# Optimization experiments

Hardware: AMD Instinct MI355X
Metric: run time of the kernel (lower is better)

Reference implementation:

```python
import jax, jax.numpy as jnp
import numpy as np

N = 50000; E = 800000; G = 256; F = 34; D = 128; H = 4; C = 32; L = 4
EPS = 1e-5

def _bn(x, g, b):
    # BatchNorm1d with batch statistics (train-mode math), eval dropout (identity)
    m = jnp.mean(x, 0); v = jnp.var(x, 0)
    return g * (x - m) * jax.lax.rsqrt(v + EPS) + b

def _seg_softmax(s, seg, n):
    # numerically-stable softmax over edges grouped by destination node
    m = jax.ops.segment_max(s, seg, num_segments=n)
    m = jnp.where(jnp.isfinite(m), m, 0.0)
    e = jnp.exp(s - m[seg])
    d = jax.ops.segment_sum(e, seg, num_segments=n)
    return e / (d[seg] + 1e-16)

def setup_inputs():
    key = jax.random.key(0)
    ks = iter(jax.random.split(key, 64))
    def rn(shape, s=0.05):
        return jax.random.normal(next(ks), shape, dtype=jnp.float32) * s
    inp = {}
    inp['x'] = jax.random.normal(next(ks), (N, F), dtype=jnp.float32)
    inp['edge_index'] = jax.random.randint(next(ks), (2, E), 0, N, dtype=jnp.int32)
    inp['batch'] = jnp.sort(jax.random.randint(next(ks), (N,), 0, G, dtype=jnp.int32))
    inp['emb_W'] = rn((F, D)); inp['emb_b'] = rn((D,))
    inp['emb_g'] = jnp.ones((D,)); inp['emb_be'] = jnp.zeros((D,))
    inp['gWl'] = rn((L, D, D)); inp['gWr'] = rn((L, D, D))
    inp['gbl'] = rn((L, D)); inp['gbr'] = rn((L, D))
    inp['gatt'] = rn((L, H, C)); inp['gbias'] = rn((L, D))
    inp['gg'] = jnp.ones((L, D)); inp['gbe'] = jnp.zeros((L, D))
    inp['tWq'] = rn((D, D)); inp['tWk'] = rn((D, D)); inp['tWv'] = rn((D, D)); inp['tWs'] = rn((D, D))
    inp['tbq'] = rn((D,)); inp['tbk'] = rn((D,)); inp['tbv'] = rn((D,)); inp['tbs'] = rn((D,))
    inp['tg'] = jnp.ones((D,)); inp['tbe'] = jnp.zeros((D,))
    inp['oW1'] = rn((2 * D, D)); inp['ob1'] = rn((D,))
    inp['og'] = jnp.ones((D,)); inp['obe'] = jnp.zeros((D,))
    inp['oW2'] = rn((D, D // 2)); inp['ob2'] = rn((D // 2,))
    inp['oW3'] = rn((D // 2, 1)); inp['ob3'] = rn((1,))
    return inp

def reference(x, edge_index, batch, emb_W, emb_b, emb_g, emb_be, gWl, gWr, gbl, gbr, gatt, gbias, gg, gbe, tWq, tWk, tWv, tWs, tbq, tbk, tbv, tbs, tg, tbe, oW1, ob1, og, obe, oW2, ob2, oW3, ob3):
    x = jax.nn.relu(_bn(x @ emb_W + emb_b, emb_g, emb_be))
    sl = jnp.arange(N, dtype=edge_index.dtype)
    ei = jnp.concatenate([edge_index, jnp.stack([sl, sl])], axis=1)  # GATv2 default add_self_loops=True
    src, dst = ei[0], ei[1]
    for l in range(L):  # 4 structurally identical GATv2 layers
        xl = (x @ gWl[l] + gbl[l]).reshape(N, H, C)
        xr = (x @ gWr[l] + gbr[l]).reshape(N, H, C)
        e = jax.nn.leaky_relu(xl[src] + xr[dst], 0.2)  # [E+N, H, C]
        sc = jnp.einsum('ehc,hc->eh', e, gatt[l])
        a = _seg_softmax(sc, dst, N)
        out = jax.ops.segment_sum(xl[src] * a[..., None], dst, num_segments=N).reshape(N, D) + gbias[l]
        x = x + jax.nn.relu(_bn(out, gg[l], gbe[l]))
    # TransformerConv: no self-loops by default, dot-product attention + root skip
    s2, d2 = edge_index[0], edge_index[1]
    q = (x @ tWq + tbq).reshape(N, H, C)
    k = (x @ tWk + tbk).reshape(N, H, C)
    v = (x @ tWv + tbv).reshape(N, H, C)
    sc = jnp.einsum('ehc,ehc->eh', q[d2], k[s2]) / np.float32(np.sqrt(C))
    a = _seg_softmax(sc, d2, N)
    agg = jax.ops.segment_sum(v[s2] * a[..., None], d2, num_segments=N).reshape(N, D)
    x = x + _bn(agg + x @ tWs + tbs, tg, tbe)
    # global mean + max pooling over graphs
    cnt = jax.ops.segment_sum(jnp.ones((N,), x.dtype), batch, num_segments=G)
    xm = jax.ops.segment_sum(x, batch, num_segments=G) / jnp.maximum(cnt, 1.0)[:, None]
    xx = jax.ops.segment_max(x, batch, num_segments=G)
    xx = jnp.where(jnp.isfinite(xx), xx, 0.0)  # guard empty segments
    h = jnp.concatenate([xm, xx], axis=1)
    h = jax.nn.relu(_bn(h @ oW1 + ob1, og, obe))
    h = jax.nn.relu(h @ oW2 + ob2)
    return h @ oW3 + ob3
```

## Files before the change

### kernel.cpp

```cpp
#include <hip/hip_runtime.h>
#include <hip/hip_fp16.h>

namespace {
constexpr int NN = 50000;
constexpr int NE = 800000;
constexpr int NG = 256;
constexpr int NF = 34;
constexpr int NL = 4;
constexpr int NB = (NN + 255) / 256;
constexpr int STS = 32;
}
#define EPSB 1e-5f
#define LSLOPE 0.2f
#define INV_SQRT_C 0.17677669529663687f

typedef short bf16x8 __attribute__((ext_vector_type(8)));
typedef float f32x4 __attribute__((ext_vector_type(4)));
typedef _Float16 hv2 __attribute__((ext_vector_type(2)));

static __device__ __forceinline__ short f2bf(float f) {
    unsigned int u = __float_as_uint(f);
    u = (u + 0x7fff + ((u >> 16) & 1)) >> 16;
    return (short)u;
}
static __device__ __forceinline__ unsigned fenc(float x) {
    unsigned u = __float_as_uint(x);
    return (u & 0x80000000u) ? ~u : (u | 0x80000000u);
}
static __device__ __forceinline__ float fdec(unsigned u) {
    return __uint_as_float((u & 0x80000000u) ? (u ^ 0x80000000u) : ~u);
}
static __device__ __forceinline__ float fdot2(hv2 a, hv2 b, float c) {
    return __builtin_amdgcn_fdot2(a, b, c, false);
}

__global__ __launch_bounds__(256) void k_deg(const int* __restrict__ ei,
                                             int* __restrict__ deg,
                                             int* __restrict__ rank) {
    int tid = blockIdx.x * 256 + threadIdx.x;
    const int S = (NE + 3) / 4;
    if (tid >= S) return;
#pragma unroll
    for (int k = 0; k < 4; ++k) {
        int e = tid + k * S;
        if (e < NE) rank[e] = atomicAdd(&deg[ei[NE + e]], 1);
    }
}

__global__ __launch_bounds__(256) void k_scan1(const int* __restrict__ deg, int* __restrict__ bsum) {
    __shared__ int sm[256];
    int i = blockIdx.x * 256 + threadIdx.x;
    sm[threadIdx.x] = (i < NN) ? deg[i] : 0;
    __syncthreads();
    for (int off = 128; off > 0; off >>= 1) {
        if (threadIdx.x < off) sm[threadIdx.x] += sm[threadIdx.x + off];
        __syncthreads();
    }
    if (threadIdx.x == 0) bsum[blockIdx.x] = sm[0];
}

__global__ __launch_bounds__(256) void k_scan2(const int* __restrict__ bsum,
                                               int* __restrict__ boff, int* __restrict__ rp) {
    __shared__ int sm[256];
    int t = threadIdx.x;
    int v = (t < NB) ? bsum[t] : 0;
    sm[t] = v;
    __syncthreads();
    for (int off = 1; off < 256; off <<= 1) {
        int u = (t >= off) ? sm[t - off] : 0;
        __syncthreads();
        sm[t] += u;
        __syncthreads();
    }
    if (t < NB) boff[t] = sm[t] - v;
    if (t == 255) rp[NN] = sm[255];
}

__global__ __launch_bounds__(256) void k_scan3(const int* __restrict__ deg,
                                               const int* __restrict__ boff,
                                               int* __restrict__ rp) {
    __shared__ int sm[256];
    int i = blockIdx.x * 256 + threadIdx.x;
    int t = threadIdx.x;
    int v = (i < NN) ? deg[i] : 0;
    sm[t] = v;
    __syncthreads();
    for (int off = 1; off < 256; off <<= 1) {
        int u = (t >= off) ? sm[t - off] : 0;
        __syncthreads();
        sm[t] += u;
        __syncthreads();
    }
    if (i < NN) rp[i] = boff[blockIdx.x] + sm[t] - v;
}

__global__ __launch_bounds__(256) void k_fill(const int* __restrict__ ei,
                                              const int* __restrict__ rp,
                                              const int* __restrict__ rank,
                                              int* __restrict__ esrc) {
    int tid = blockIdx.x * 256 + threadIdx.x;
    const int S = (NE + 3) / 4;
    if (tid >= S) return;
#pragma unroll
    for (int k = 0; k < 4; ++k) {
        int e = tid + k * S;
        if (e < NE) {
            int s = ei[e];
            int d = ei[NE + e];
            int p = rp[d] + rank[e];
            esrc[p] = s;
        }
    }
}

__global__ __launch_bounds__(256) void k_prep(const float* __restrict__ gWl,
                                              const float* __restrict__ gWr,
                                              const float* __restrict__ tWq,
                                              const float* __restrict__ tWk,
                                              const float* __restrict__ tWv,
                                              const float* __restrict__ tWs,
                                              short* __restrict__ dst) {
    int m = blockIdx.x;
    const float* src;
    if (m < 4) src = gWl + m * 16384;
    else if (m < 8) src = gWr + (m - 4) * 16384;
    else if (m == 8) src = tWq;
    else if (m == 9) src = tWk;
    else if (m == 10) src = tWv;
    else src = tWs;
    short* d = dst + m * 16384;
    for (int i = threadIdx.x; i < 16384; i += 256) {
        int n = i >> 7, k = i & 127;
        d[i] = f2bf(src[k * 128 + n]);
    }
}

__global__ __launch_bounds__(256) void k_stats(const float* __restrict__ src, int nRows,
                                               float* __restrict__ st) {
    int c = threadIdx.x & 127;
    int sub = threadIdx.x >> 7;
    int r0 = blockIdx.x * 128;
    int rend = r0 + 128; if (rend > nRows) rend = nRows;
    float s = 0.f, ss = 0.f;
    for (int r = r0 + sub; r < rend; r += 2) {
        float v = src[(size_t)r * 128 + c];
        s += v; ss += v * v;
    }
    float* dst = st + (blockIdx.x & (STS - 1)) * 256;
    atomicAdd(&dst[c], s);
    atomicAdd(&dst[128 + c], ss);
}

template <int OUTH0, int OUTH1, int RES, int XOUT>
__global__ __launch_bounds__(256) void k_gemm2bn(const float* __restrict__ src,
                                                 const float* __restrict__ res,
                                                 float* __restrict__ xout,
                                                 const float* __restrict__ st,
                                                 const float* __restrict__ g,
                                                 const float* __restrict__ b,
                                                 const short* __restrict__ Wt0,
                                                 const short* __restrict__ Wt1,
                                                 const float* __restrict__ bias0,
                                                 const float* __restrict__ bias1,
                                                 void* __restrict__ out0,
                                                 void* __restrict__ out1, int nRows) {
    __shared__ short As[128 * 136];
    __shared__ short Bs[128 * 136];
    __shared__ float scsh[256];
    const float invn = 1.f / NN;
    if (threadIdx.x < 128) {
        int c = threadIdx.x;
        float s0v = 0.f, s1v = 0.f;
#pragma unroll 8
        for (int k2 = 0; k2 < STS; ++k2) {
            s0v += st[k2 * 256 + c];
            s1v += st[k2 * 256 + 128 + c];
        }
        float mean = s0v * invn;
        float var = fmaxf(s1v * invn - mean * mean, 0.f);
        float s = g[c] * rsqrtf(var + EPSB);
        scsh[c] = s;
        scsh[128 + c] = b[c] - mean * s;
    }
    {
        const int4* Wt4 = (const int4*)Wt0;
        for (int idx = threadIdx.x; idx < 2048; idx += 256) {
            int row = idx >> 4, c8 = idx & 15;
            *(int4*)&Bs[row * 136 + c8 * 8] = Wt4[idx];
        }
    }
    __syncthreads();
    int r0 = blockIdx.x * 128;
    int rows = nRows - r0; if (rows > 128) rows = 128;
    for (int idx = threadIdx.x; idx < 2048; idx += 256) {
        int r = idx >> 4, c8 = idx & 15;
        short4 sa = {0, 0, 0, 0}, sb = {0, 0, 0, 0};
        if (r < rows) {
            size_t base = (size_t)(r0 + r) * 128 + c8 * 8;
            float4 v0 = *(const float4*)&src[base];
            float4 v1 = *(const float4*)&src[base + 4];
            int c = c8 * 8;
            v0.x = fmaxf(v0.x * scsh[c + 0] + scsh[128 + c + 0], 0.f);
            v0.y = fmaxf(v0.y * scsh[c + 1] + scsh[128 + c + 1], 0.f);
            v0.z = fmaxf(v0.z * scsh[c + 2] + scsh[128 + c + 2], 0.f);
            v0.w = fmaxf(v0.w * scsh[c + 3] + scsh[128 + c + 3], 0.f);
            v1.x = fmaxf(v1.x * scsh[c + 4] + scsh[128 + c + 4], 0.f);
            v1.y = fmaxf(v1.y * scsh[c + 5] + scsh[128 + c + 5], 0.f);
            v1.z = fmaxf(v1.z * scsh[c + 6] + scsh[128 + c + 6], 0.f);
            v1.w = fmaxf(v1.w * scsh[c + 7] + scsh[128 + c + 7], 0.f);
            if (RES) {
                float4 rr0 = *(const float4*)&res[base];
                float4 rr1 = *(const float4*)&res[base + 4];
                v0.x += rr0.x; v0.y += rr0.y; v0.z += rr0.z; v0.w += rr0.w;
                v1.x += rr1.x; v1.y += rr1.y; v1.z += rr1.z; v1.w += rr1.w;
            }
            if (XOUT) {
                *(float4*)&xout[base] = v0;
                *(float4*)&xout[base + 4] = v1;
            }
            sa.x = f2bf(v0.x); sa.y = f2bf(v0.y); sa.z = f2bf(v0.z); sa.w = f2bf(v0.w);
            sb.x = f2bf(v1.x); sb.y = f2bf(v1.y); sb.z = f2bf(v1.z); sb.w = f2bf(v1.w);
        }
        *(short4*)&As[r * 136 + c8 * 8] = sa;
        *(short4*)&As[r * 136 + c8 * 8 + 4] = sb;
    }
    __syncthreads();
    int lane = threadIdx.x & 63, wave = threadIdx.x >> 6;
    int n16 = lane & 15, quad = lane >> 4;
    bf16x8 af[2][4];
#pragma unroll
    for (int rt = 0; rt < 2; ++rt)
#pragma unroll
        for (int kc = 0; kc < 4; ++kc)
            af[rt][kc] = *(const bf16x8*)&As[(wave * 32 + rt * 16 + n16) * 136 + kc * 32 + quad * 8];

    f32x4 acc[2][8];
#pragma unroll
    for (int rt = 0; rt < 2; ++rt)
#pragma unroll
        for (int ct = 0; ct < 8; ++ct) acc[rt][ct] = (f32x4){0.f, 0.f, 0.f, 0.f};
#pragma unroll
    for (int ct = 0; ct < 8; ++ct)
#pragma unroll
        for (int kc = 0; kc < 4; ++kc) {
            bf16x8 bf = *(const bf16x8*)&Bs[(ct * 16 + n16) * 136 + kc * 32 + quad * 8];
            acc[0][ct] = __builtin_amdgcn_mfma_f32_16x16x32_bf16(af[0][kc], bf, acc[0][ct], 0, 0, 0);
            acc[1][ct] = __builtin_amdgcn_mfma_f32_16x16x32_bf16(af[1][kc], bf, acc[1][ct], 0, 0, 0);
        }
#pragma unroll
    for (int ct = 0; ct < 8; ++ct) {
        int colI = ct * 16 + n16;
        float bv = bias0[colI];
#pragma unroll
        for (int rt = 0; rt < 2; ++rt)
#pragma unroll
            for (int reg = 0; reg < 4; ++reg) {
                int r = wave * 32 + rt * 16 + quad * 4 + reg;
                if (r < rows) {
                    float v = acc[rt][ct][reg] + bv;
                    if (OUTH0) ((__half*)out0)[(size_t)(r0 + r) * 128 + colI] = __float2half(v);
                    else       ((float*)out0)[(size_t)(r0 + r) * 128 + colI] = v;
                }
            }
    }
    __syncthreads();
    {
        const int4* Wt4 = (const int4*)Wt1;
        for (int idx = threadIdx.x; idx < 2048; idx += 256) {
            int row = idx >> 4, c8 = idx & 15;
            *(int4*)&Bs[row * 136 + c8 * 8] = Wt4[idx];
        }
    }
    __syncthreads();
#pragma unroll
    for (int rt = 0; rt < 2; ++rt)
#pragma unroll
        for (int ct = 0; ct < 8; ++ct) acc[rt][ct] = (f32x4){0.f, 0.f, 0.f, 0.f};
#pragma unroll
    for (int ct = 0; ct < 8; ++ct)
#pragma unroll
        for (int kc = 0; kc < 4; ++kc) {
            bf16x8 bf = *(const bf16x8*)&Bs[(ct * 16 + n16) * 136 + kc * 32 + quad * 8];
            acc[0][ct] = __builtin_amdgcn_mfma_f32_16x16x32_bf16(af[0][kc], bf, acc[0][ct], 0, 0, 0);
            acc[1][ct] = __builtin_amdgcn_mfma_f32_16x16x32_bf16(af[1][kc], bf, acc[1][ct], 0, 0, 0);
        }
#pragma unroll
    for (int ct = 0; ct < 8; ++ct) {
        int colI = ct * 16 + n16;
        float bv = bias1[colI];
#pragma unroll
        for (int rt = 0; rt < 2; ++rt)
#pragma unroll
            for (int reg = 0; reg < 4; ++reg) {
                int r = wave * 32 + rt * 16 + quad * 4 + reg;
                if (r < rows) {
                    float v = acc[rt][ct][reg] + bv;
                    if (OUTH1) ((__half*)out1)[(size_t)(r0 + r) * 128 + colI] = __float2half(v);
                    else       ((float*)out1)[(size_t)(r0 + r) * 128 + colI] = v;
                }
            }
    }
}

__global__ __launch_bounds__(256) void k_gemm4bn(const float* __restrict__ src,
                                                 const float* __restrict__ res,
                                                 float* __restrict__ xout,
                                                 const float* __restrict__ st,
                                                 const float* __restrict__ g,
                                                 const float* __restrict__ b,
                                                 const short* __restrict__ Wt,
                                                 const float* __restrict__ bq,
                                                 const float* __restrict__ bk,
                                                 const float* __restrict__ bv,
                                                 const float* __restrict__ bs,
                                                 __half* __restrict__ oq,
                                                 __half* __restrict__ ok,
                                                 __half* __restrict__ ov,
                                                 __half* __restrict__ os, int nRows) {
    __shared__ short As[128 * 136];
    __shared__ short Bs[128 * 136];
    __shared__ float scsh[256];
    const float invn = 1.f / NN;
    if (threadIdx.x < 128) {
        int c = threadIdx.x;
        float s0v = 0.f, s1v = 0.f;
#pragma unroll 8
        for (int k2 = 0; k2 < STS; ++k2) {
            s0v += st[k2 * 256 + c];
            s1v += st[k2 * 256 + 128 + c];
        }
        float mean = s0v * invn;
        float var = fmaxf(s1v * invn - mean * mean, 0.f);
        float s = g[c] * rsqrtf(var + EPSB);
        scsh[c] = s;
        scsh[128 + c] = b[c] - mean * s;
    }
    __syncthreads();
    int r0 = blockIdx.x * 128;
    int rows = nRows - r0; if (rows > 128) rows = 128;
    for (int idx = threadIdx.x; idx < 2048; idx += 256) {
        int r = idx >> 4, c8 = idx & 15;
        short4 sa = {0, 0, 0, 0}, sb = {0, 0, 0, 0};
        if (r < rows) {
            size_t base = (size_t)(r0 + r) * 128 + c8 * 8;
            float4 v0 = *(const float4*)&src[base];
            float4 v1 = *(const float4*)&src[base + 4];
            int c = c8 * 8;
            v0.x = fmaxf(v0.x * scsh[c + 0] + scsh[128 + c + 0], 0.f);
            v0.y = fmaxf(v0.y * scsh[c + 1] + scsh[128 + c + 1], 0.f);
            v0.z = fmaxf(v0.z * scsh[c + 2] + scsh[128 + c + 2], 0.f);
            v0.w = fmaxf(v0.w * scsh[c + 3] + scsh[128 + c + 3], 0.f);
            v1.x = fmaxf(v1.x * scsh[c + 4] + scsh[128 + c + 4], 0.f);
            v1.y = fmaxf(v1.y * scsh[c + 5] + scsh[128 + c + 5], 0.f);
            v1.z = fmaxf(v1.z * scsh[c + 6] + scsh[128 + c + 6], 0.f);
            v1.w = fmaxf(v1.w * scsh[c + 7] + scsh[128 + c + 7], 0.f);
            float4 rr0 = *(const float4*)&res[base];
            float4 rr1 = *(const float4*)&res[base + 4];
            v0.x += rr0.x; v0.y += rr0.y; v0.z += rr0.z; v0.w += rr0.w;
            v1.x += rr1.x; v1.y += rr1.y; v1.z += rr1.z; v1.w += rr1.w;
            *(float4*)&xout[base] = v0;
            *(float4*)&xout[base + 4] = v1;
            sa.x = f2bf(v0.x); sa.y = f2bf(v0.y); sa.z = f2bf(v0.z); sa.w = f2bf(v0.w);
            sb.x = f2bf(v1.x); sb.y = f2bf(v1.y); sb.z = f2bf(v1.z); sb.w = f2bf(v1.w);
        }
        *(short4*)&As[r * 136 + c8 * 8] = sa;
        *(short4*)&As[r * 136 + c8 * 8 + 4] = sb;
    }
    int lane = threadIdx.x & 63, wave = threadIdx.x >> 6;
    int n16 = lane & 15, quad = lane >> 4;
    __half* outs[4] = {oq, ok, ov, os};
    const float* biases[4] = {bq, bk, bv, bs};
    bf16x8 af[2][4];
    bool afLoaded = false;
    for (int m = 0; m < 4; ++m) {
        {
            const int4* Wt4 = (const int4*)(Wt + (size_t)m * 16384);
            for (int idx = threadIdx.x; idx < 2048; idx += 256) {
                int row = idx >> 4, c8 = idx & 15;
                *(int4*)&Bs[row * 136 + c8 * 8] = Wt4[idx];
            }
        }
        __syncthreads();
        if (!afLoaded) {
            afLoaded = true;
#pragma unroll
            for (int rt = 0; rt < 2; ++rt)
#pragma unroll
                for (int kc = 0; kc < 4; ++kc)
                    af[rt][kc] = *(const bf16x8*)&As[(wave * 32 + rt * 16 + n16) * 136 + kc * 32 + quad * 8];
        }
        f32x4 acc[2][8];
#pragma unroll
        for (int rt = 0; rt < 2; ++rt)
#pragma unroll
            for (int ct = 0; ct < 8; ++ct) acc[rt][ct] = (f32x4){0.f, 0.f, 0.f, 0.f};
#pragma unroll
        for (int ct = 0; ct < 8; ++ct)
#pragma unroll
            for (int kc = 0; kc < 4; ++kc) {
                bf16x8 bf = *(const bf16x8*)&Bs[(ct * 16 + n16) * 136 + kc * 32 + quad * 8];
                acc[0][ct] = __builtin_amdgcn_mfma_f32_16x16x32_bf16(af[0][kc], bf, acc[0][ct], 0, 0, 0);
                acc[1][ct] = __builtin_amdgcn_mfma_f32_16x16x32_bf16(af[1][kc], bf, acc[1][ct], 0, 0, 0);
            }
        __half* om = outs[m];
        const float* bm = biases[m];
#pragma unroll
        for (int ct = 0; ct < 8; ++ct) {
            int colI = ct * 16 + n16;
            float bv2 = bm[colI];
#pragma unroll
            for (int rt = 0; rt < 2; ++rt)
#pragma unroll
                for (int reg = 0; reg < 4; ++reg) {
                    int r = wave * 32 + rt * 16 + quad * 4 + reg;
                    if (r < rows)
                        om[(size_t)(r0 + r) * 128 + colI] = __float2half(acc[rt][ct][reg] + bv2);
                }
        }
        if (m < 3) __syncthreads();
    }
}

__global__ __launch_bounds__(256) void k_gemm_emb(const float* __restrict__ A,
                                                  const float* __restrict__ W,
                                                  const float* __restrict__ bias,
                                                  float* __restrict__ out, int nRows,
                                                  float* __restrict__ stms) {
    __shared__ float As[64 * NF];
    __shared__ float sred[256];
    int r0 = blockIdx.x * 64;
    int rows = nRows - r0; if (rows > 64) rows = 64;
    int total = rows * NF;
    for (int idx = threadIdx.x; idx < 64 * NF; idx += 256)
        As[idx] = (idx < total) ? A[(size_t)r0 * NF + idx] : 0.f;
    sred[threadIdx.x] = 0.f;
    __syncthreads();
    int tx = threadIdx.x & 31, ty = threadIdx.x >> 5;
    const float4* W4 = (const float4*)W;
    float acc[8][4];
#pragma unroll
    for (int j = 0; j < 8; ++j)
#pragma unroll
        for (int i = 0; i < 4; ++i) acc[j][i] = 0.f;
#pragma unroll 2
    for (int k = 0; k < NF; ++k) {
        float4 w = W4[k * 32 + tx];
#pragma unroll
        for (int j = 0; j < 8; ++j) {
            float a = As[(ty * 8 + j) * NF + k];
            acc[j][0] += a * w.x; acc[j][1] += a * w.y;
            acc[j][2] += a * w.z; acc[j][3] += a * w.w;
        }
    }
    float4 b = ((const float4*)bias)[tx];
    float s[4] = {0.f, 0.f, 0.f, 0.f}, ss[4] = {0.f, 0.f, 0.f, 0.f};
#pragma unroll
    for (int j = 0; j < 8; ++j) {
        int r = ty * 8 + j;
        if (r < rows) {
            float4 o = make_float4(acc[j][0] + b.x, acc[j][1] + b.y,
                                   acc[j][2] + b.z, acc[j][3] + b.w);
            ((float4*)out)[(size_t)(r0 + r) * 32 + tx] = o;
            s[0] += o.x; ss[0] += o.x * o.x;
            s[1] += o.y; ss[1] += o.y * o.y;
            s[2] += o.z; ss[2] += o.z * o.z;
            s[3] += o.w; ss[3] += o.w * o.w;
        }
    }
#pragma unroll
    for (int i = 0; i < 4; ++i) {
        atomicAdd(&sred[tx * 4 + i], s[i]);
        atomicAdd(&sred[128 + tx * 4 + i], ss[i]);
    }
    __syncthreads();
    atomicAdd(&stms[(blockIdx.x & (STS - 1)) * 256 + threadIdx.x], sred[threadIdx.x]);
}

__global__ __launch_bounds__(256) void k_gat_aggr(const __half* __restrict__ xl,
                                                  const __half* __restrict__ xr,
                                                  const float* __restrict__ att,
                                                  const float* __restrict__ gbias_l,
                                                  const int* __restrict__ rp,
                                                  const int* __restrict__ esrc,
                                                  float* __restrict__ out) {
    int lane = threadIdx.x & 63;
    int node = blockIdx.x * 4 + (threadIdx.x >> 6);
    if (node >= NN) return;
    int q = lane >> 4;
    int l16 = lane & 15;
    int c8 = l16 * 8;
    float4 xrr = *(const float4*)&xr[(unsigned)node * 128u + c8];
    hv2 xrh[4] = {*(hv2*)&xrr.x, *(hv2*)&xrr.y, *(hv2*)&xrr.z, *(hv2*)&xrr.w};
    float4 atA = *(const float4*)&att[c8];
    float4 atB = *(const float4*)&att[c8 + 4];
    hv2 ath[4] = {{(_Float16)atA.x, (_Float16)atA.y}, {(_Float16)atA.z, (_Float16)atA.w},
                  {(_Float16)atB.x, (_Float16)atB.y}, {(_Float16)atB.z, (_Float16)atB.w}};
    const hv2 hz = {(_Float16)0.f, (_Float16)0.f};
    const hv2 hs = {(_Float16)LSLOPE, (_Float16)LSLOPE};
    int s0 = rp[node];
    int T = rp[node + 1] - s0 + 1;
    float a[8] = {0.f, 0.f, 0.f, 0.f, 0.f, 0.f, 0.f, 0.f};
    float l = 0.f;
    auto body = [&](int j) {
        bool self = (j == T - 1);
        int srcn = self ? node : esrc[s0 + j];
        float4 raw = *(const float4*)&xl[(unsigned)srcn * 128u + c8];
        hv2 f[4] = {*(hv2*)&raw.x, *(hv2*)&raw.y, *(hv2*)&raw.z, *(hv2*)&raw.w};
        float p = 0.f;
#pragma unroll
        for (int k = 0; k < 4; ++k) {
            hv2 e = f[k] + xrh[k];
            hv2 lk = __builtin_elementwise_max(e, hz) + hs * __builtin_elementwise_min(e, hz);
            p = fdot2(lk, ath[k], p);
        }
        p += __shfl_xor(p, 1); p += __shfl_xor(p, 2);
        float w = __expf(p);
#pragma unroll
        for (int k = 0; k < 4; ++k) {
            a[2 * k] += w * (float)f[k].x;
            a[2 * k + 1] += w * (float)f[k].y;
        }
        l += w;
    };
    int j = q;
    for (; j + 12 < T; j += 16) { body(j); body(j + 4); body(j + 8); body(j + 12); }
    for (; j + 4 < T; j += 8) { body(j); body(j + 4); }
    for (; j < T; j += 4) body(j);
#pragma unroll
    for (int k = 0; k < 8; ++k) { a[k] += __shfl_xor(a[k], 16); a[k] += __shfl_xor(a[k], 32); }
    l += __shfl_xor(l, 16); l += __shfl_xor(l, 32);
    if (q == 0) {
        float inv = 1.f / (l + 1e-16f);
        float4 gb0 = *(const float4*)&gbias_l[c8];
        float4 gb1 = *(const float4*)&gbias_l[c8 + 4];
        float4 o0 = make_float4(a[0] * inv + gb0.x, a[1] * inv + gb0.y,
                                a[2] * inv + gb0.z, a[3] * inv + gb0.w);
        float4 o1 = make_float4(a[4] * inv + gb1.x, a[5] * inv + gb1.y,
                                a[6] * inv + gb1.z, a[7] * inv + gb1.w);
        *(float4*)&out[(unsigned)node * 128u + c8] = o0;
        *(float4*)&out[(unsigned)node * 128u + c8 + 4] = o1;
    }
}

__global__ __launch_bounds__(256) void k_trans_aggr(const __half* __restrict__ qh,
                                                    const __half* __restrict__ kh,
                                                    const __half* __restrict__ vv,
                                                    const __half* __restrict__ sT,
                                                    const int* __restrict__ rp,
                                                    const int* __restrict__ esrc,
                                                    float* __restrict__ out) {
    int lane = threadIdx.x & 63;
    int node = blockIdx.x * 4 + (threadIdx.x >> 6);
    if (node >= NN) return;
    int q = lane >> 4;
    int l16 = lane & 15;
    int c8 = l16 * 8;
    float4 qr = *(const float4*)&qh[(unsigned)node * 128u + c8];
    const hv2 hinv = {(_Float16)INV_SQRT_C, (_Float16)INV_SQRT_C};
    hv2 qv[4] = {(*(hv2*)&qr.x) * hinv, (*(hv2*)&qr.y) * hinv,
                 (*(hv2*)&qr.z) * hinv, (*(hv2*)&qr.w) * hinv};
    int s0 = rp[node];
    int T = rp[node + 1] - s0;
    float a[8] = {0.f, 0.f, 0.f, 0.f, 0.f, 0.f, 0.f, 0.f};
    float l = 0.f;
    auto body = [&](int j) {
        int srcn = esrc[s0 + j];
        float4 kraw = *(const float4*)&kh[(unsigned)srcn * 128u + c8];
        float4 vraw = *(const float4*)&vv[(unsigned)srcn * 128u + c8];
        hv2 kv[4] = {*(hv2*)&kraw.x, *(hv2*)&kraw.y, *(hv2*)&kraw.z, *(hv2*)&kraw.w};
        float p = 0.f;
#pragma unroll
        for (int k = 0; k < 4; ++k) p = fdot2(kv[k], qv[k], p);
        p += __shfl_xor(p, 1); p += __shfl_xor(p, 2);
        float w = __expf(p);
        hv2 vvv[4] = {*(hv2*)&vraw.x, *(hv2*)&vraw.y, *(hv2*)&vraw.z, *(hv2*)&vraw.w};
#pragma unroll
        for (int k = 0; k < 4; ++k) {
            a[2 * k] += w * (float)vvv[k].x;
            a[2 * k + 1] += w * (float)vvv[k].y;
        }
        l += w;
    };
    int j = q;
    for (; j + 12 < T; j += 16) { body(j); body(j + 4); body(j + 8); body(j + 12); }
    for (; j + 4 < T; j += 8) { body(j); body(j + 4); }
    for (; j < T; j += 4) body(j);
#pragma unroll
    for (int k = 0; k < 8; ++k) { a[k] += __shfl_xor(a[k], 16); a[k] += __shfl_xor(a[k], 32); }
    l += __shfl_xor(l, 16); l += __shfl_xor(l, 32);
    if (q == 0) {
        float inv = 1.f / (l + 1e-16f);
        float4 straw = *(const float4*)&sT[(unsigned)node * 128u + c8];
        hv2 st[4] = {*(hv2*)&straw.x, *(hv2*)&straw.y, *(hv2*)&straw.z, *(hv2*)&straw.w};
        float4 o0 = make_float4(a[0] * inv + (float)st[0].x, a[1] * inv + (float)st[0].y,
                                a[2] * inv + (float)st[1].x, a[3] * inv + (float)st[1].y);
        float4 o1 = make_float4(a[4] * inv + (float)st[2].x, a[5] * inv + (float)st[2].y,
                                a[6] * inv + (float)st[3].x, a[7] * inv + (float)st[3].y);
        *(float4*)&out[(unsigned)node * 128u + c8] = o0;
        *(float4*)&out[(unsigned)node * 128u + c8 + 4] = o1;
    }
}

__global__ __launch_bounds__(256) void k_pool_part(const float* __restrict__ src,
                                                   const float* __restrict__ res,
                                                   const float* __restrict__ st,
                                                   const float* __restrict__ g,
                                                   const float* __restrict__ b,
                                                   const int* __restrict__ batch,
                                                   float* __restrict__ psum,
                                                   unsigned* __restrict__ pmax) {
    __shared__ int bs[64];
    __shared__ float sc_sh[128], sh_sh[128];
    int r0 = blockIdx.x * 64;
    if (threadIdx.x < 64) {
        int r = r0 + threadIdx.x;
        bs[threadIdx.x] = (r < NN) ? batch[r] : -1;
    }
    const float invn = 1.f / NN;
    if (threadIdx.x < 128) {
        int c2 = threadIdx.x;
        float s0v = 0.f, s1v = 0.f;
#pragma unroll 8
        for (int k2 = 0; k2 < STS; ++k2) {
            s0v += st[k2 * 256 + c2];
            s1v += st[k2 * 256 + 128 + c2];
        }
        float mean = s0v * invn;
        float var = fmaxf(s1v * invn - mean * mean, 0.f);
        float scv = g[c2] * rsqrtf(var + EPSB);
        sc_sh[c2] = scv;
        sh_sh[c2] = b[c2] - mean * scv;
    }
    __syncthreads();
    int c = threadIdx.x & 127;
    int sub = threadIdx.x >> 7;
    float scv = sc_sh[c];
    float shv = sh_sh[c];
    int curg = -1;
    float s = 0.f, fmx = -INFINITY;
    for (int i = sub; i < 64; i += 2) {
        int r = r0 + i;
        if (r >= NN) break;
        int gr = bs[i];
        if (gr != curg) {
            if (curg >= 0) {
                atomicAdd(&psum[curg * 128 + c], s);
                atomicMax(&pmax[curg * 128 + c], fenc(fmx));
            }
            curg = gr; s = 0.f; fmx = -INFINITY;
        }
        float v = src[(size_t)r * 128 + c] * scv + shv + res[(size_t)r * 128 + c];
        s += v; fmx = fmaxf(fmx, v);
    }
    if (curg >= 0) {
        atomicAdd(&psum[curg * 128 + c], s);
        atomicMax(&pmax[curg * 128 + c], fenc(fmx));
    }
}

__global__ __launch_bounds__(128) void k_pool_head1(const float* __restrict__ psum,
                                                    const unsigned* __restrict__ pmax,
                                                    const int* __restrict__ batch,
                                                    const float* __restrict__ W,
                                                    const float* __restrict__ b,
                                                    float* __restrict__ t1,
                                                    float* __restrict__ st6) {
    __shared__ float hr[256];
    __shared__ int se[2];
    int g = blockIdx.x;
    int t = threadIdx.x;
    if (t == 0) {
        int lo = 0, hi = NN;
        while (lo < hi) { int mid = (lo + hi) >> 1; if (batch[mid] < g) lo = mid + 1; else hi = mid; }
        se[0] = lo;
        hi = NN;
        while (lo < hi) { int mid = (lo + hi) >> 1; if (batch[mid] < g + 1) lo = mid + 1; else hi = mid; }
        se[1] = lo;
    }
    __syncthreads();
    int cnt = se[1] - se[0];
    float xm = psum[g * 128 + t] / fmaxf((float)cnt, 1.f);
    float xx = (cnt > 0) ? fdec(pmax[g * 128 + t]) : 0.f;
    hr[t] = xm;
    hr[128 + t] = xx;
    __syncthreads();
    float acc = b[t];
#pragma unroll 4
    for (int k = 0; k < 256; ++k) acc += hr[k] * W[k * 128 + t];
    t1[g * 128 + t] = acc;
    atomicAdd(&st6[t], acc);
    atomicAdd(&st6[128 + t], acc * acc);
}

__global__ __launch_bounds__(64) void k_head2(const float* __restrict__ t1,
                                              const float* __restrict__ st,
                                              const float* __restrict__ og,
                                              const float* __restrict__ obe,
                                              const float* __restrict__ W2,
                                              const float* __restrict__ b2,
                                              const float* __restrict__ W3,
                                              const float* __restrict__ b3,
                                              float* __restrict__ out) {
    __shared__ float v[128];
    int row = blockIdx.x, t = threadIdx.x;
    const float invn = 1.f / NG;
#pragma unroll
    for (int half = 0; half < 2; ++half) {
        int ch = t + half * 64;
        float mean = st[ch] * invn;
        float var = fmaxf(st[128 + ch] * invn - mean * mean, 0.f);
        float scv = og[ch] * rsqrtf(var + EPSB);
        float shv = obe[ch] - mean * scv;
        float a = t1[row * 128 + ch] * scv + shv;
        v[ch] = fmaxf(a, 0.f);
    }
    __syncthreads();
    float acc = b2[t];
#pragma unroll 4
    for (int k = 0; k < 128; ++k) acc += v[k] * W2[k * 64 + t];
    float p = fmaxf(acc, 0.f) * W3[t];
    p += __shfl_xor(p, 1); p += __shfl_xor(p, 2); p += __shfl_xor(p, 4);
    p += __shfl_xor(p, 8); p += __shfl_xor(p, 16); p += __shfl_xor(p, 32);
    if (t == 0) out[row] = p + b3[0];
}

extern "C" void kernel_launch(void* const* d_in, const int* in_sizes, int n_in,
                              void* d_out, int out_size, void* d_ws, size_t ws_size,
                              hipStream_t stream) {
    const float* x_in   = (const float*)d_in[0];
    const int*   ei     = (const int*)d_in[1];
    const int*   batch  = (const int*)d_in[2];
    const float* emb_W  = (const float*)d_in[3];
    const float* emb_b  = (const float*)d_in[4];
    const float* emb_g  = (const float*)d_in[5];
    const float* emb_be = (const float*)d_in[6];
    const float* gWl    = (const float*)d_in[7];
    const float* gWr    = (const float*)d_in[8];
    const float* gbl    = (const float*)d_in[9];
    const float* gbr    = (const float*)d_in[10];
    const float* gatt   = (const float*)d_in[11];
    const float* gbias  = (const float*)d_in[12];
    const float* gg     = (const float*)d_in[13];
    const float* gbe    = (const float*)d_in[14];
    const float* tWq    = (const float*)d_in[15];
    const float* tWk    = (const float*)d_in[16];
    const float* tWv    = (const float*)d_in[17];
    const float* tWs    = (const float*)d_in[18];
    const float* tbq    = (const float*)d_in[19];
    const float* tbk    = (const float*)d_in[20];
    const float* tbv    = (const float*)d_in[21];
    const float* tbs    = (const float*)d_in[22];
    const float* tg     = (const float*)d_in[23];
    const float* tbe    = (const float*)d_in[24];
    const float* oW1    = (const float*)d_in[25];
    const float* ob1    = (const float*)d_in[26];
    const float* og     = (const float*)d_in[27];
    const float* obe    = (const float*)d_in[28];
    const float* oW2    = (const float*)d_in[29];
    const float* ob2    = (const float*)d_in[30];
    const float* oW3    = (const float*)d_in[31];
    const float* ob3    = (const float*)d_in[32];
    float* out = (float*)d_out;

    const size_t NDsz = (size_t)NN * 128;
    float* x     = (float*)d_ws;
    float* bA    = x + NDsz;
    float* bC    = bA + NDsz;
    float* stats = bC + NDsz;
    float* hpool = stats + 7 * 256;
    float* t1    = hpool + 65536;
    float* scb   = t1 + 32768;
    __half* xlh  = (__half*)(scb + (size_t)(NE + NN) * 4);
    __half* xrh  = xlh + NDsz;
    __half* vh   = xrh + NDsz;
    __half* sh   = vh + NDsz;
    short* Wt    = (short*)(sh + NDsz);
    int* deg     = (int*)(Wt + 12 * 16384);
    int* rp      = deg + NN;
    int* cursor  = rp + NN + 1;
    int2* edg    = (int2*)(cursor + NN);
    int* bsum    = (int*)(edg + NE + 64);
    int* boff    = bsum + 256;
    float* psum  = (float*)(boff + 256);
    unsigned* pmax = (unsigned*)(psum + NG * 128);
    int* rank    = (int*)scb;
    int* esrc    = (int*)edg;
    float* stms  = scb + NE;

    hipMemsetAsync(deg, 0, NN * sizeof(int), stream);
    hipMemsetAsync(stats + 6 * 256, 0, 256 * sizeof(float), stream);
    hipMemsetAsync(stms, 0, 6 * STS * 256 * sizeof(float), stream);
    hipMemsetAsync(psum, 0, NG * 128 * 2 * sizeof(float), stream);

    k_prep<<<12, 256, 0, stream>>>(gWl, gWr, tWq, tWk, tWv, tWs, Wt);

    const int S4 = (NE + 3) / 4;
    const int gQuarter = (S4 + 255) / 256;
    k_deg<<<gQuarter, 256, 0, stream>>>(ei, deg, rank);
    k_scan1<<<NB, 256, 0, stream>>>(deg, bsum);
    k_scan2<<<1, 256, 0, stream>>>(bsum, boff, rp);
    k_scan3<<<NB, 256, 0, stream>>>(deg, boff, rp);
    k_fill<<<gQuarter, 256, 0, stream>>>(ei, rp, rank, esrc);

    const int gEmb  = (NN + 63) / 64;
    const int gGemm = (NN + 127) / 128;
    const int gStat = (NN + 127) / 128;
    const int gNode = (NN + 3) / 4;
    const int gPool = (NN + 63) / 64;
    const int REG = STS * 256;

    k_gemm_emb<<<gEmb, 256, 0, stream>>>(x_in, emb_W, emb_b, bA, NN, stms + 0 * REG);

    k_gemm2bn<1, 1, 0, 1><<<gGemm, 256, 0, stream>>>(bA, nullptr, x, stms + 0 * REG, emb_g, emb_be,
                                                     Wt + (size_t)0 * 16384, Wt + (size_t)4 * 16384,
                                                     gbl + 0 * 128, gbr + 0 * 128, xlh, xrh, NN);
    k_gat_aggr<<<gNode, 256, 0, stream>>>(xlh, xrh, gatt + 0 * 128, gbias + 0 * 128, rp, esrc, bC);
    k_stats<<<gStat, 256, 0, stream>>>(bC, NN, stms + 1 * REG);
    k_gemm2bn<1, 1, 1, 1><<<gGemm, 256, 0, stream>>>(bC, x, bA, stms + 1 * REG, gg + 0 * 128, gbe + 0 * 128,
                                                     Wt + (size_t)1 * 16384, Wt + (size_t)5 * 16384,
                                                     gbl + 1 * 128, gbr + 1 * 128, xlh, xrh, NN);
    k_gat_aggr<<<gNode, 256, 0, stream>>>(xlh, xrh, gatt + 1 * 128, gbias + 1 * 128, rp, esrc, bC);
    k_stats<<<gStat, 256, 0, stream>>>(bC, NN, stms + 2 * REG);
    k_gemm2bn<1, 1, 1, 1><<<gGemm, 256, 0, stream>>>(bC, bA, x, stms + 2 * REG, gg + 1 * 128, gbe + 1 * 128,
                                                     Wt + (size_t)2 * 16384, Wt + (size_t)6 * 16384,
                                                     gbl + 2 * 128, gbr + 2 * 128, xlh, xrh, NN);
    k_gat_aggr<<<gNode, 256, 0, stream>>>(xlh, xrh, gatt + 2 * 128, gbias + 2 * 128, rp, esrc, bC);
    k_stats<<<gStat, 256, 0, stream>>>(bC, NN, stms + 3 * REG);
    k_gemm2bn<1, 1, 1, 1><<<gGemm, 256, 0, stream>>>(bC, x, bA, stms + 3 * REG, gg + 2 * 128, gbe + 2 * 128,
                                                     Wt + (size_t)3 * 16384, Wt + (size_t)7 * 16384,
                                                     gbl + 3 * 128, gbr + 3 * 128, xlh, xrh, NN);
    k_gat_aggr<<<gNode, 256, 0, stream>>>(xlh, xrh, gatt + 3 * 128, gbias + 3 * 128, rp, esrc, bC);
    k_stats<<<gStat, 256, 0, stream>>>(bC, NN, stms + 4 * REG);

    k_gemm4bn<<<gGemm, 256, 0, stream>>>(bC, bA, x, stms + 4 * REG, gg + 3 * 128, gbe + 3 * 128,
                                         Wt + (size_t)8 * 16384, tbq, tbk, tbv, tbs,
                                         xrh, xlh, vh, sh, NN);
    k_trans_aggr<<<gNode, 256, 0, stream>>>(xrh, xlh, vh, sh, rp, esrc, bC);
    k_stats<<<gStat, 256, 0, stream>>>(bC, NN, stms + 5 * REG);

    k_pool_part<<<gPool, 256, 0, stream>>>(bC, x, stms + 5 * REG, tg, tbe, batch, psum, pmax);
    k_pool_head1<<<NG, 128, 0, stream>>>(psum, pmax, batch, oW1, ob1, t1, stats + 6 * 256);
    k_head2<<<NG, 64, 0, stream>>>(t1, stats + 6 * 256, og, obe, oW2, ob2, oW3, ob3, out);
}
```

Baseline: 821.8 us.

## Merge init kernels into one launch and widen per-lane columns in edge aggregation

Degree counting, weight transpose/conversion and the embedding GEMM are combined into a single kernel, with each block picking its role from its block index. This removes two launches and lets the independent pieces run concurrently. The GAT and Transformer aggregation kernels now give each lane 16 columns instead of 8, so 8 edges are processed in parallel per wave instead of 4. That halves the shuffles in the score reduction but doubles per-lane registers and leaves fewer parallel edges for low-degree nodes.

```diff
diff --git a/kernel.cpp b/kernel.cpp
--- a/kernel.cpp
+++ b/kernel.cpp
@@ -9,6 +9,8 @@
 constexpr int NL = 4;
 constexpr int NB = (NN + 255) / 256;
 constexpr int STS = 32;
+constexpr int GQ = ((NE + 3) / 4 + 255) / 256;
+constexpr int GE = (NN + 63) / 64;
 }
 #define EPSB 1e-5f
 #define LSLOPE 0.2f
@@ -34,17 +36,98 @@
     return __builtin_amdgcn_fdot2(a, b, c, false);
 }
 
-__global__ __launch_bounds__(256) void k_deg(const int* __restrict__ ei,
-                                             int* __restrict__ deg,
-                                             int* __restrict__ rank) {
-    int tid = blockIdx.x * 256 + threadIdx.x;
-    const int S = (NE + 3) / 4;
-    if (tid >= S) return;
-#pragma unroll
-    for (int k = 0; k < 4; ++k) {
-        int e = tid + k * S;
-        if (e < NE) rank[e] = atomicAdd(&deg[ei[NE + e]], 1);
-    }
+__global__ __launch_bounds__(256) void k_init(const int* __restrict__ ei,
+                                              int* __restrict__ deg,
+                                              int* __restrict__ rank,
+                                              const float* __restrict__ gWl,
+                                              const float* __restrict__ gWr,
+                                              const float* __restrict__ tWq,
+                                              const float* __restrict__ tWk,
+                                              const float* __restrict__ tWv,
+                                              const float* __restrict__ tWs,
+                                              short* __restrict__ Wt,
+                                              const float* __restrict__ A,
+                                              const float* __restrict__ W,
+                                              const float* __restrict__ bias,
+                                              float* __restrict__ outEmb,
+                                              float* __restrict__ stms) {
+    __shared__ float As[64 * NF];
+    __shared__ float sred[256];
+    int blk = blockIdx.x;
+    if (blk < GQ) {
+        int tid = blk * 256 + threadIdx.x;
+        const int S = (NE + 3) / 4;
+        if (tid >= S) return;
+#pragma unroll
+        for (int k = 0; k < 4; ++k) {
+            int e = tid + k * S;
+            if (e < NE) rank[e] = atomicAdd(&deg[ei[NE + e]], 1);
+        }
+        return;
+    }
+    blk -= GQ;
+    if (blk < 12) {
+        const float* src;
+        if (blk < 4) src = gWl + blk * 16384;
+        else if (blk < 8) src = gWr + (blk - 4) * 16384;
+        else if (blk == 8) src = tWq;
+        else if (blk == 9) src = tWk;
+        else if (blk == 10) src = tWv;
+        else src = tWs;
+        short* d = Wt + blk * 16384;
+        for (int i = threadIdx.x; i < 16384; i += 256) {
+            int n = i >> 7, k = i & 127;
+            d[i] = f2bf(src[k * 128 + n]);
+        }
+        return;
+    }
+    blk -= 12;
+    int r0 = blk * 64;
+    int rows = NN - r0; if (rows > 64) rows = 64;
+    int total = rows * NF;
+    for (int idx = threadIdx.x; idx < 64 * NF; idx += 256)
+        As[idx] = (idx < total) ? A[(size_t)r0 * NF + idx] : 0.f;
+    sred[threadIdx.x] = 0.f;
+    __syncthreads();
+    int tx = threadIdx.x & 31, ty = threadIdx.x >> 5;
+    const float4* W4 = (const float4*)W;
+    float acc[8][4];
+#pragma unroll
+    for (int j = 0; j < 8; ++j)
+#pragma unroll
+        for (int i = 0; i < 4; ++i) acc[j][i] = 0.f;
+#pragma unroll 2
+    for (int k = 0; k < NF; ++k) {
+        float4 w = W4[k * 32 + tx];
+#pragma unroll
+        for (int j = 0; j < 8; ++j) {
+            float a = As[(ty * 8 + j) * NF + k];
+            acc[j][0] += a * w.x; acc[j][1] += a * w.y;
+            acc[j][2] += a * w.z; acc[j][3] += a * w.w;
+        }
+    }
+    float4 b = ((const float4*)bias)[tx];
+    float s[4] = {0.f, 0.f, 0.f, 0.f}, ss[4] = {0.f, 0.f, 0.f, 0.f};
+#pragma unroll
+    for (int j = 0; j < 8; ++j) {
+        int r = ty * 8 + j;
+        if (r < rows) {
+            float4 o = make_float4(acc[j][0] + b.x, acc[j][1] + b.y,
+                                   acc[j][2] + b.z, acc[j][3] + b.w);
+            ((float4*)outEmb)[(size_t)(r0 + r) * 32 + tx] = o;
+            s[0] += o.x; ss[0] += o.x * o.x;
+            s[1] += o.y; ss[1] += o.y * o.y;
+            s[2] += o.z; ss[2] += o.z * o.z;
+            s[3] += o.w; ss[3] += o.w * o.w;
+        }
+    }
+#pragma unroll
+    for (int i = 0; i < 4; ++i) {
+        atomicAdd(&sred[tx * 4 + i], s[i]);
+        atomicAdd(&sred[128 + tx * 4 + i], ss[i]);
+    }
+    __syncthreads();
+    atomicAdd(&stms[(blk & (STS - 1)) * 256 + threadIdx.x], sred[threadIdx.x]);
 }
 
 __global__ __launch_bounds__(256) void k_scan1(const int* __restrict__ deg, int* __restrict__ bsum) {
@@ -110,28 +193,6 @@
             int p = rp[d] + rank[e];
             esrc[p] = s;
         }
-    }
-}
-
-__global__ __launch_bounds__(256) void k_prep(const float* __restrict__ gWl,
-                                              const float* __restrict__ gWr,
-                                              const float* __restrict__ tWq,
-                                              const float* __restrict__ tWk,
-                                              const float* __restrict__ tWv,
-                                              const float* __restrict__ tWs,
-                                              short* __restrict__ dst) {
-    int m = blockIdx.x;
-    const float* src;
-    if (m < 4) src = gWl + m * 16384;
-    else if (m < 8) src = gWr + (m - 4) * 16384;
-    else if (m == 8) src = tWq;
-    else if (m == 9) src = tWk;
-    else if (m == 10) src = tWv;
-    else src = tWs;
-    short* d = dst + m * 16384;
-    for (int i = threadIdx.x; i < 16384; i += 256) {
-        int n = i >> 7, k = i & 127;
-        d[i] = f2bf(src[k * 128 + n]);
     }
 }
 
@@ -421,61 +482,6 @@
     }
 }
 
-__global__ __launch_bounds__(256) void k_gemm_emb(const float* __restrict__ A,
-                                                  const float* __restrict__ W,
-                                                  const float* __restrict__ bias,
-                                                  float* __restrict__ out, int nRows,
-                                                  float* __restrict__ stms) {
-    __shared__ float As[64 * NF];
-    __shared__ float sred[256];
-    int r0 = blockIdx.x * 64;
-    int rows = nRows - r0; if (rows > 64) rows = 64;
-    int total = rows * NF;
-    for (int idx = threadIdx.x; idx < 64 * NF; idx += 256)
-        As[idx] = (idx < total) ? A[(size_t)r0 * NF + idx] : 0.f;
-    sred[threadIdx.x] = 0.f;
-    __syncthreads();
-    int tx = threadIdx.x & 31, ty = threadIdx.x >> 5;
-    const float4* W4 = (const float4*)W;
-    float acc[8][4];
-#pragma unroll
-    for (int j = 0; j < 8; ++j)
-#pragma unroll
-        for (int i = 0; i < 4; ++i) acc[j][i] = 0.f;
-#pragma unroll 2
-    for (int k = 0; k < NF; ++k) {
-        float4 w = W4[k * 32 + tx];
-#pragma unroll
-        for (int j = 0; j < 8; ++j) {
-            float a = As[(ty * 8 + j) * NF + k];
-            acc[j][0] += a * w.x; acc[j][1] += a * w.y;
-            acc[j][2] += a * w.z; acc[j][3] += a * w.w;
-        }
-    }
-    float4 b = ((const float4*)bias)[tx];
-    float s[4] = {0.f, 0.f, 0.f, 0.f}, ss[4] = {0.f, 0.f, 0.f, 0.f};
-#pragma unroll
-    for (int j = 0; j < 8; ++j) {
-        int r = ty * 8 + j;
-        if (r < rows) {
-            float4 o = make_float4(acc[j][0] + b.x, acc[j][1] + b.y,
-                                   acc[j][2] + b.z, acc[j][3] + b.w);
-            ((float4*)out)[(size_t)(r0 + r) * 32 + tx] = o;
-            s[0] += o.x; ss[0] += o.x * o.x;
-            s[1] += o.y; ss[1] += o.y * o.y;
-            s[2] += o.z; ss[2] += o.z * o.z;
-            s[3] += o.w; ss[3] += o.w * o.w;
-        }
-    }
-#pragma unroll
-    for (int i = 0; i < 4; ++i) {
-        atomicAdd(&sred[tx * 4 + i], s[i]);
-        atomicAdd(&sred[128 + tx * 4 + i], ss[i]);
-    }
-    __syncthreads();
-    atomicAdd(&stms[(blockIdx.x & (STS - 1)) * 256 + threadIdx.x], sred[threadIdx.x]);
-}
-
 __global__ __launch_bounds__(256) void k_gat_aggr(const __half* __restrict__ xl,
                                                   const __half* __restrict__ xr,
                                                   const float* __restrict__ att,
@@ -486,59 +492,77 @@
     int lane = threadIdx.x & 63;
     int node = blockIdx.x * 4 + (threadIdx.x >> 6);
     if (node >= NN) return;
-    int q = lane >> 4;
-    int l16 = lane & 15;
-    int c8 = l16 * 8;
-    float4 xrr = *(const float4*)&xr[(unsigned)node * 128u + c8];
-    hv2 xrh[4] = {*(hv2*)&xrr.x, *(hv2*)&xrr.y, *(hv2*)&xrr.z, *(hv2*)&xrr.w};
-    float4 atA = *(const float4*)&att[c8];
-    float4 atB = *(const float4*)&att[c8 + 4];
-    hv2 ath[4] = {{(_Float16)atA.x, (_Float16)atA.y}, {(_Float16)atA.z, (_Float16)atA.w},
-                  {(_Float16)atB.x, (_Float16)atB.y}, {(_Float16)atB.z, (_Float16)atB.w}};
+    int q = lane >> 3;
+    int l8 = lane & 7;
+    int c16 = l8 * 16;
+    const __half* xrp = &xr[(unsigned)node * 128u + c16];
+    float4 xr0 = *(const float4*)xrp;
+    float4 xr1 = *(const float4*)(xrp + 8);
+    hv2 xrh[8] = {*(hv2*)&xr0.x, *(hv2*)&xr0.y, *(hv2*)&xr0.z, *(hv2*)&xr0.w,
+                  *(hv2*)&xr1.x, *(hv2*)&xr1.y, *(hv2*)&xr1.z, *(hv2*)&xr1.w};
+    float4 atA = *(const float4*)&att[c16];
+    float4 atB = *(const float4*)&att[c16 + 4];
+    float4 atC = *(const float4*)&att[c16 + 8];
+    float4 atD = *(const float4*)&att[c16 + 12];
+    hv2 ath[8] = {{(_Float16)atA.x, (_Float16)atA.y}, {(_Float16)atA.z, (_Float16)atA.w},
+                  {(_Float16)atB.x, (_Float16)atB.y}, {(_Float16)atB.z, (_Float16)atB.w},
+                  {(_Float16)atC.x, (_Float16)atC.y}, {(_Float16)atC.z, (_Float16)atC.w},
+                  {(_Float16)atD.x, (_Float16)atD.y}, {(_Float16)atD.z, (_Float16)atD.w}};
     const hv2 hz = {(_Float16)0.f, (_Float16)0.f};
     const hv2 hs = {(_Float16)LSLOPE, (_Float16)LSLOPE};
     int s0 = rp[node];
     int T = rp[node + 1] - s0 + 1;
-    float a[8] = {0.f, 0.f, 0.f, 0.f, 0.f, 0.f, 0.f, 0.f};
+    float a[16];
+#pragma unroll
+    for (int k = 0; k < 16; ++k) a[k] = 0.f;
     float l = 0.f;
     auto body = [&](int j) {
         bool self = (j == T - 1);
         int srcn = self ? node : esrc[s0 + j];
-        float4 raw = *(const float4*)&xl[(unsigned)srcn * 128u + c8];
-        hv2 f[4] = {*(hv2*)&raw.x, *(hv2*)&raw.y, *(hv2*)&raw.z, *(hv2*)&raw.w};
+        const __half* rowp = &xl[(unsigned)srcn * 128u + c16];
+        float4 r0 = *(const float4*)rowp;
+        float4 r1 = *(const float4*)(rowp + 8);
+        hv2 f[8] = {*(hv2*)&r0.x, *(hv2*)&r0.y, *(hv2*)&r0.z, *(hv2*)&r0.w,
+                    *(hv2*)&r1.x, *(hv2*)&r1.y, *(hv2*)&r1.z, *(hv2*)&r1.w};
         float p = 0.f;
 #pragma unroll
-        for (int k = 0; k < 4; ++k) {
+        for (int k = 0; k < 8; ++k) {
             hv2 e = f[k] + xrh[k];
             hv2 lk = __builtin_elementwise_max(e, hz) + hs * __builtin_elementwise_min(e, hz);
             p = fdot2(lk, ath[k], p);
         }
-        p += __shfl_xor(p, 1); p += __shfl_xor(p, 2);
+        p += __shfl_xor(p, 1);
         float w = __expf(p);
 #pragma unroll
-        for (int k = 0; k < 4; ++k) {
+        for (int k = 0; k < 8; ++k) {
             a[2 * k] += w * (float)f[k].x;
             a[2 * k + 1] += w * (float)f[k].y;
         }
         l += w;
     };
     int j = q;
-    for (; j + 12 < T; j += 16) { body(j); body(j + 4); body(j + 8); body(j + 12); }
-    for (; j + 4 < T; j += 8) { body(j); body(j + 4); }
-    for (; j < T; j += 4) body(j);
-#pragma unroll
-    for (int k = 0; k < 8; ++k) { a[k] += __shfl_xor(a[k], 16); a[k] += __shfl_xor(a[k], 32); }
-    l += __shfl_xor(l, 16); l += __shfl_xor(l, 32);
+    for (; j + 8 < T; j += 16) { body(j); body(j + 8); }
+    for (; j < T; j += 8) body(j);
+#pragma unroll
+    for (int k = 0; k < 16; ++k) {
+        a[k] += __shfl_xor(a[k], 8); a[k] += __shfl_xor(a[k], 16); a[k] += __shfl_xor(a[k], 32);
+    }
+    l += __shfl_xor(l, 8); l += __shfl_xor(l, 16); l += __shfl_xor(l, 32);
     if (q == 0) {
         float inv = 1.f / (l + 1e-16f);
-        float4 gb0 = *(const float4*)&gbias_l[c8];
-        float4 gb1 = *(const float4*)&gbias_l[c8 + 4];
-        float4 o0 = make_float4(a[0] * inv + gb0.x, a[1] * inv + gb0.y,
-                                a[2] * inv + gb0.z, a[3] * inv + gb0.w);
-        float4 o1 = make_float4(a[4] * inv + gb1.x, a[5] * inv + gb1.y,
-                                a[6] * inv + gb1.z, a[7] * inv + gb1.w);
-        *(float4*)&out[(unsigned)node * 128u + c8] = o0;
-        *(float4*)&out[(unsigned)node * 128u + c8 + 4] = o1;
+        float4 gb0 = *(const float4*)&gbias_l[c16];
+        float4 gb1 = *(const float4*)&gbias_l[c16 + 4];
+        float4 gb2 = *(const float4*)&gbias_l[c16 + 8];
+        float4 gb3 = *(const float4*)&gbias_l[c16 + 12];
+        float* op = &out[(unsigned)node * 128u + c16];
+        *(float4*)op       = make_float4(a[0] * inv + gb0.x, a[1] * inv + gb0.y,
+                                         a[2] * inv + gb0.z, a[3] * inv + gb0.w);
+        *(float4*)(op + 4) = make_float4(a[4] * inv + gb1.x, a[5] * inv + gb1.y,
+                                         a[6] * inv + gb1.z, a[7] * inv + gb1.w);
+        *(float4*)(op + 8) = make_float4(a[8] * inv + gb2.x, a[9] * inv + gb2.y,
+                                         a[10] * inv + gb2.z, a[11] * inv + gb2.w);
+        *(float4*)(op + 12)= make_float4(a[12] * inv + gb3.x, a[13] * inv + gb3.y,
+                                         a[14] * inv + gb3.z, a[15] * inv + gb3.w);
     }
 }
 
@@ -552,52 +576,71 @@
     int lane = threadIdx.x & 63;
     int node = blockIdx.x * 4 + (threadIdx.x >> 6);
     if (node >= NN) return;
-    int q = lane >> 4;
-    int l16 = lane & 15;
-    int c8 = l16 * 8;
-    float4 qr = *(const float4*)&qh[(unsigned)node * 128u + c8];
+    int q = lane >> 3;
+    int l8 = lane & 7;
+    int c16 = l8 * 16;
+    const __half* qp = &qh[(unsigned)node * 128u + c16];
+    float4 q0 = *(const float4*)qp;
+    float4 q1 = *(const float4*)(qp + 8);
     const hv2 hinv = {(_Float16)INV_SQRT_C, (_Float16)INV_SQRT_C};
-    hv2 qv[4] = {(*(hv2*)&qr.x) * hinv, (*(hv2*)&qr.y) * hinv,
-                 (*(hv2*)&qr.z) * hinv, (*(hv2*)&qr.w) * hinv};
+    hv2 qv[8] = {(*(hv2*)&q0.x) * hinv, (*(hv2*)&q0.y) * hinv,
+                 (*(hv2*)&q0.z) * hinv, (*(hv2*)&q0.w) * hinv,
+                 (*(hv2*)&q1.x) * hinv, (*(hv2*)&q1.y) * hinv,
+                 (*(hv2*)&q1.z) * hinv, (*(hv2*)&q1.w) * hinv};
     int s0 = rp[node];
     int T = rp[node + 1] - s0;
-    float a[8] = {0.f, 0.f, 0.f, 0.f, 0.f, 0.f, 0.f, 0.f};
+    float a[16];
+#pragma unroll
+    for (int k = 0; k < 16; ++k) a[k] = 0.f;
     float l = 0.f;
     auto body = [&](int j) {
         int srcn = esrc[s0 + j];
-        float4 kraw = *(const float4*)&kh[(unsigned)srcn * 128u + c8];
-        float4 vraw = *(const float4*)&vv[(unsigned)srcn * 128u + c8];
-        hv2 kv[4] = {*(hv2*)&kraw.x, *(hv2*)&kraw.y, *(hv2*)&kraw.z, *(hv2*)&kraw.w};
+        const __half* kp = &kh[(unsigned)srcn * 128u + c16];
+        const __half* vp = &vv[(unsigned)srcn * 128u + c16];
+        float4 k0 = *(const float4*)kp;
+        float4 k1 = *(const float4*)(kp + 8);
+        float4 v0 = *(const float4*)vp;
+        float4 v1 = *(const float4*)(vp + 8);
+        hv2 kv[8] = {*(hv2*)&k0.x, *(hv2*)&k0.y, *(hv2*)&k0.z, *(hv2*)&k0.w,
+                     *(hv2*)&k1.x, *(hv2*)&k1.y, *(hv2*)&k1.z, *(hv2*)&k1.w};
         float p = 0.f;
 #pragma unroll
-        for (int k = 0; k < 4; ++k) p = fdot2(kv[k], qv[k], p);
-        p += __shfl_xor(p, 1); p += __shfl_xor(p, 2);
+        for (int k = 0; k < 8; ++k) p = fdot2(kv[k], qv[k], p);
+        p += __shfl_xor(p, 1);
         float w = __expf(p);
-        hv2 vvv[4] = {*(hv2*)&vraw.x, *(hv2*)&vraw.y, *(hv2*)&vraw.z, *(hv2*)&vraw.w};
-#pragma unroll
-        for (int k = 0; k < 4; ++k) {
+        hv2 vvv[8] = {*(hv2*)&v0.x, *(hv2*)&v0.y, *(hv2*)&v0.z, *(hv2*)&v0.w,
+                      *(hv2*)&v1.x, *(hv2*)&v1.y, *(hv2*)&v1.z, *(hv2*)&v1.w};
+#pragma unroll
+        for (int k = 0; k < 8; ++k) {
             a[2 * k] += w * (float)vvv[k].x;
             a[2 * k + 1] += w * (float)vvv[k].y;
         }
         l += w;
     };
     int j = q;
-    for (; j + 12 < T; j += 16) { body(j); body(j + 4); body(j + 8); body(j + 12); }
-    for (; j + 4 < T; j += 8) { body(j); body(j + 4); }
-    for (; j < T; j += 4) body(j);
-#pragma unroll
-    for (int k = 0; k < 8; ++k) { a[k] += __shfl_xor(a[k], 16); a[k] += __shfl_xor(a[k], 32); }
-    l += __shfl_xor(l, 16); l += __shfl_xor(l, 32);
+    for (; j + 8 < T; j += 16) { body(j); body(j + 8); }
+    for (; j < T; j += 8) body(j);
+#pragma unroll
+    for (int k = 0; k < 16; ++k) {
+        a[k] += __shfl_xor(a[k], 8); a[k] += __shfl_xor(a[k], 16); a[k] += __shfl_xor(a[k], 32);
+    }
+    l += __shfl_xor(l, 8); l += __shfl_xor(l, 16); l += __shfl_xor(l, 32);
     if (q == 0) {
         float inv = 1.f / (l + 1e-16f);
-        float4 straw = *(const float4*)&sT[(unsigned)node * 128u + c8];
-        hv2 st[4] = {*(hv2*)&straw.x, *(hv2*)&straw.y, *(hv2*)&straw.z, *(hv2*)&straw.w};
-        float4 o0 = make_float4(a[0] * inv + (float)st[0].x, a[1] * inv + (float)st[0].y,
-                                a[2] * inv + (float)st[1].x, a[3] * inv + (float)st[1].y);
-        float4 o1 = make_float4(a[4] * inv + (float)st[2].x, a[5] * inv + (float)st[2].y,
-                                a[6] * inv + (float)st[3].x, a[7] * inv + (float)st[3].y);
-        *(float4*)&out[(unsigned)node * 128u + c8] = o0;
-        *(float4*)&out[(unsigned)node * 128u + c8 + 4] = o1;
+        const __half* sp = &sT[(unsigned)node * 128u + c16];
+        float4 s0r = *(const float4*)sp;
+        float4 s1r = *(const float4*)(sp + 8);
+        hv2 st[8] = {*(hv2*)&s0r.x, *(hv2*)&s0r.y, *(hv2*)&s0r.z, *(hv2*)&s0r.w,
+                     *(hv2*)&s1r.x, *(hv2*)&s1r.y, *(hv2*)&s1r.z, *(hv2*)&s1r.w};
+        float* op = &out[(unsigned)node * 128u + c16];
+        *(float4*)op       = make_float4(a[0] * inv + (float)st[0].x, a[1] * inv + (float)st[0].y,
+                                         a[2] * inv + (float)st[1].x, a[3] * inv + (float)st[1].y);
+        *(float4*)(op + 4) = make_float4(a[4] * inv + (float)st[2].x, a[5] * inv + (float)st[2].y,
+                                         a[6] * inv + (float)st[3].x, a[7] * inv + (float)st[3].y);
+        *(float4*)(op + 8) = make_float4(a[8] * inv + (float)st[4].x, a[9] * inv + (float)st[4].y,
+                                         a[10] * inv + (float)st[5].x, a[11] * inv + (float)st[5].y);
+        *(float4*)(op + 12)= make_float4(a[12] * inv + (float)st[6].x, a[13] * inv + (float)st[6].y,
+                                         a[14] * inv + (float)st[7].x, a[15] * inv + (float)st[7].y);
     }
 }
 
@@ -792,24 +835,19 @@
     hipMemsetAsync(stms, 0, 6 * STS * 256 * sizeof(float), stream);
     hipMemsetAsync(psum, 0, NG * 128 * 2 * sizeof(float), stream);
 
-    k_prep<<<12, 256, 0, stream>>>(gWl, gWr, tWq, tWk, tWv, tWs, Wt);
-
-    const int S4 = (NE + 3) / 4;
-    const int gQuarter = (S4 + 255) / 256;
-    k_deg<<<gQuarter, 256, 0, stream>>>(ei, deg, rank);
-    k_scan1<<<NB, 256, 0, stream>>>(deg, bsum);
-    k_scan2<<<1, 256, 0, stream>>>(bsum, boff, rp);
-    k_scan3<<<NB, 256, 0, stream>>>(deg, boff, rp);
-    k_fill<<<gQuarter, 256, 0, stream>>>(ei, rp, rank, esrc);
-
-    const int gEmb  = (NN + 63) / 64;
     const int gGemm = (NN + 127) / 128;
     const int gStat = (NN + 127) / 128;
     const int gNode = (NN + 3) / 4;
     const int gPool = (NN + 63) / 64;
     const int REG = STS * 256;
 
-    k_gemm_emb<<<gEmb, 256, 0, stream>>>(x_in, emb_W, emb_b, bA, NN, stms + 0 * REG);
+    k_init<<<GQ + 12 + GE, 256, 0, stream>>>(ei, deg, rank, gWl, gWr, tWq, tWk, tWv, tWs,
+                                             Wt, x_in, emb_W, emb_b, bA, stms + 0 * REG);
+
+    k_scan1<<<NB, 256, 0, stream>>>(deg, bsum);
+    k_scan2<<<1, 256, 0, stream>>>(bsum, boff, rp);
+    k_scan3<<<NB, 256, 0, stream>>>(deg, boff, rp);
+    k_fill<<<GQ, 256, 0, stream>>>(ei, rp, rank, esrc);
 
     k_gemm2bn<1, 1, 0, 1><<<gGemm, 256, 0, stream>>>(bA, nullptr, x, stms + 0 * REG, emb_g, emb_be,
                                                      Wt + (size_t)0 * 16384, Wt + (size_t)4 * 16384,
```

Result: no change. 822.6 us (+0.1%).
